# Kernel tuning notes

Hardware: AMD Instinct MI355X
Metric: run time of the kernel (lower is better)

Reference implementation:

```python
import jax, jax.numpy as jnp
import numpy as np

EMBED_DIM = 1024
BATCH = 4
SEQ = 2048


def setup_inputs() -> dict:
    key = jax.random.key(0)
    ks = jax.random.split(key, 9)
    E = EMBED_DIM
    s = 1.0 / np.sqrt(E)
    inp = {
        "x": jax.random.normal(ks[0], (BATCH, SEQ, E), dtype=jnp.float32),
        "Wq": jax.random.uniform(ks[1], (E, E), jnp.float32, -s, s),
        "bq": jax.random.uniform(ks[2], (E,), jnp.float32, -s, s),
        "Wk": jax.random.uniform(ks[3], (E, E), jnp.float32, -s, s),
        "bk": jax.random.uniform(ks[4], (E,), jnp.float32, -s, s),
        "Wv": jax.random.uniform(ks[5], (E, E), jnp.float32, -s, s),
        "bv": jax.random.uniform(ks[6], (E,), jnp.float32, -s, s),
        "Wo": jax.random.uniform(ks[7], (E, E), jnp.float32, -s, s),
        "bo": jax.random.uniform(ks[8], (E,), jnp.float32, -s, s),
    }
    return inp


def reference(x, Wq, bq, Wk, bk, Wv, bv, Wo, bo):
    # x: [B, S, E]. Single-head attention over full embed_dim.
    scale = x.shape[-1] ** -0.5
    q = jnp.einsum("bse,ef->bsf", x, Wq.T) + bq
    k = jnp.einsum("bse,ef->bsf", x, Wk.T) + bk
    v = jnp.einsum("bse,ef->bsf", x, Wv.T) + bv
    scores = jnp.einsum("bqe,bke->bqk", q, k) * scale  # [B, S, S]
    attn = jax.nn.softmax(scores, axis=-1)             # dropout p=0 -> identity
    out = jnp.einsum("bqk,bke->bqe", attn, v)
    return jnp.einsum("bse,ef->bsf", out, Wo.T) + bo
```

## Files before the change

### kernel.cpp

```cpp
#include <hip/hip_runtime.h>
#include <hip/hip_bf16.h>


typedef __bf16 bf16_t;
typedef __bf16 bf16x8 __attribute__((ext_vector_type(8)));
typedef __bf16 bf16x4 __attribute__((ext_vector_type(4)));
typedef float  f32x16 __attribute__((ext_vector_type(16)));
typedef float  f32x4  __attribute__((ext_vector_type(4)));

__device__ __forceinline__ void async_copy16(const void* g, void* l) {
  __builtin_amdgcn_global_load_lds(
      (const __attribute__((address_space(1))) void*)g,
      (__attribute__((address_space(3))) void*)l, 16, 0, 0);
}

__device__ __forceinline__ void wg_barrier() {
  asm volatile("" ::: "memory");
  __builtin_amdgcn_s_barrier();
  asm volatile("" ::: "memory");
}

#define LGKM(n)                                                  \
  do {                                                           \
    asm volatile("s_waitcnt lgkmcnt(" #n ")" ::: "memory");      \
    __builtin_amdgcn_sched_barrier(0);                           \
  } while (0)

#define VM(n) asm volatile("s_waitcnt vmcnt(" #n ")" ::: "memory")

__device__ __forceinline__ unsigned lds_addr(const void* p) {
  return (unsigned)(unsigned long long)(__attribute__((address_space(3))) const void*)p;
}

__device__ __forceinline__ bf16x8 ds_read128(const bf16_t* p) {
  bf16x8 r;
  asm volatile("ds_read_b128 %0, %1" : "=v"(r) : "v"(lds_addr(p)));
  return r;
}

__device__ __forceinline__ f32x4 mfma16(bf16x8 a, bf16x8 b, f32x4 c) {
  return __builtin_amdgcn_mfma_f32_16x16x32_bf16(a, b, c, 0, 0, 0);
}

__device__ __forceinline__ void store_out(float* p, float v)  { *p = v; }
__device__ __forceinline__ void store_out(bf16_t* p, float v) { *p = (bf16_t)v; }

#define BM 128
#define BN 128
#define BKT 64

#define G_AQ(i, ro, bb, co)                                                   \
  acc[(ro) + (i)][(co) + 0] = mfma16(a[i][0], bb[0][0], acc[(ro) + (i)][(co) + 0]); \
  acc[(ro) + (i)][(co) + 1] = mfma16(a[i][0], bb[1][0], acc[(ro) + (i)][(co) + 1]); \
  acc[(ro) + (i)][(co) + 0] = mfma16(a[i][1], bb[0][1], acc[(ro) + (i)][(co) + 0]); \
  acc[(ro) + (i)][(co) + 1] = mfma16(a[i][1], bb[1][1], acc[(ro) + (i)][(co) + 1]);

#define G_BQ(j, bb, co)                                              \
  acc[0][(co) + (j)] = mfma16(a[0][0], bb[j][0], acc[0][(co) + (j)]); \
  acc[1][(co) + (j)] = mfma16(a[1][0], bb[j][0], acc[1][(co) + (j)]); \
  acc[2][(co) + (j)] = mfma16(a[2][0], bb[j][0], acc[2][(co) + (j)]); \
  acc[3][(co) + (j)] = mfma16(a[3][0], bb[j][0], acc[3][(co) + (j)]); \
  acc[0][(co) + (j)] = mfma16(a[0][1], bb[j][1], acc[0][(co) + (j)]); \
  acc[1][(co) + (j)] = mfma16(a[1][1], bb[j][1], acc[1][(co) + (j)]); \
  acc[2][(co) + (j)] = mfma16(a[2][1], bb[j][1], acc[2][(co) + (j)]); \
  acc[3][(co) + (j)] = mfma16(a[3][1], bb[j][1], acc[3][(co) + (j)]);

template <typename OutT, int NBIAS>
__global__ __launch_bounds__(512, 2) void gemm256_bt(
    const bf16_t* __restrict__ A, const bf16_t* __restrict__ B,
    OutT* __restrict__ C,
    const float* __restrict__ b0, const float* __restrict__ b1,
    const float* __restrict__ b2,
    int M, int N, int K, int lda, int ldb, int ldc, float scale,
    long long strideA, long long strideB, long long strideC) {
  const int z = blockIdx.z;
  A += (long long)z * strideA;
  B += (long long)z * strideB;
  C += (long long)z * strideC;

  int bx = blockIdx.x, by = blockIdx.y;
  {
    const int GX  = gridDim.x;
    const int id  = by * GX + bx;
    const int per = GX * 8;
    const int grp = id / per;
    const int rem = id - grp * per;
    by = grp * 8 + (rem & 7);
    bx = rem >> 3;
  }

  __shared__ __align__(16) bf16_t As[2 * 256 * 64];
  __shared__ __align__(16) bf16_t Bs[2 * 256 * 64];

  const int t    = threadIdx.x;
  const int lane = t & 63;
  const int w    = t >> 6;
  const int wm   = w & 1;
  const int wn   = w >> 1;
  const int g    = lane >> 4;
  const int l7   = lane & 7;
  const int r15  = lane & 15;
  const int tileM = by * 256;
  const int tileN = bx * 256;

  const int row0 = t >> 3;
  const int gcc  = (t & 7) ^ (row0 & 7);
  const int dstb = (t & ~63) * 8;

  const int sw0 = ((0 + g) ^ l7) * 8;
  const int sw1 = ((4 + g) ^ l7) * 8;
  const int aRow = (wm * 128 + r15) * 64;
  const int bRow = (wn * 64 + r15) * 64;

  const int NT = K >> 6;

  f32x4 acc[8][4] = {};

  auto stageA = [&](int kt, int h) {
    const int cb = (kt & 1) * 16384;
    const bf16_t* src =
        A + (long long)(tileM + h * 128 + row0) * lda + kt * 64 + gcc * 8;
    bf16_t* dst = &As[cb + h * 8192 + dstb];
    async_copy16(src, dst);
    async_copy16(src + (long long)64 * lda, dst + 4096);
  };
  auto stageB = [&](int kt, int h) {
    const int cb = (kt & 1) * 16384;
    const bf16_t* src =
        B + (long long)(tileN + h * 128 + row0) * ldb + kt * 64 + gcc * 8;
    bf16_t* dst = &Bs[cb + h * 8192 + dstb];
    async_copy16(src, dst);
    async_copy16(src + (long long)64 * ldb, dst + 4096);
  };

  stageA(0, 0); stageA(0, 1); stageB(0, 0); stageB(0, 1);
  VM(0);
  wg_barrier();

  bf16x8 a[4][2], P[2][2], Q[2][2];
#pragma unroll
  for (int j = 0; j < 2; ++j) {
    P[j][0] = ds_read128(&Bs[bRow + j * 1024 + sw0]);
    P[j][1] = ds_read128(&Bs[bRow + j * 1024 + sw1]);
  }

  auto tile_step = [&](int kt, bf16x8 (&bc)[2][2], bf16x8 (&bq)[2][2]) {
    const int cb = (kt & 1) * 16384;
    const int kn = kt + 1;
    const bf16_t* Ab = &As[cb + aRow];
    const bf16_t* Bb = &Bs[cb + bRow];

#pragma unroll
    for (int i = 0; i < 4; ++i) {
      a[i][0] = ds_read128(Ab + i * 1024 + sw0);
      a[i][1] = ds_read128(Ab + i * 1024 + sw1);
    }
    if (kn < NT) { stageB(kn, 0); stageB(kn, 1); }
    __builtin_amdgcn_s_setprio(1);
    LGKM(6);
    G_AQ(0, 0, bc, 0)
    LGKM(4);
    G_AQ(1, 0, bc, 0)
    LGKM(2);
    G_AQ(2, 0, bc, 0)
    LGKM(0);
    G_AQ(3, 0, bc, 0)
    __builtin_amdgcn_s_setprio(0);

#pragma unroll
    for (int j = 0; j < 2; ++j) {
      bq[j][0] = ds_read128(Bb + 2048 + j * 1024 + sw0);
      bq[j][1] = ds_read128(Bb + 2048 + j * 1024 + sw1);
    }
    if (kn < NT) { stageA(kn, 0); stageA(kn, 1); }
    __builtin_amdgcn_s_setprio(1);
    LGKM(2);
    G_BQ(0, bq, 2)
    LGKM(0);
    G_BQ(1, bq, 2)
    __builtin_amdgcn_s_setprio(0);

#pragma unroll
    for (int i = 0; i < 4; ++i) {
      a[i][0] = ds_read128(Ab + 4096 + i * 1024 + sw0);
      a[i][1] = ds_read128(Ab + 4096 + i * 1024 + sw1);
    }
    __builtin_amdgcn_s_setprio(1);
    LGKM(6);
    G_AQ(0, 4, bq, 2)
    LGKM(4);
    G_AQ(1, 4, bq, 2)
    LGKM(2);
    G_AQ(2, 4, bq, 2)
    LGKM(0);
    G_AQ(3, 4, bq, 2)
    __builtin_amdgcn_s_setprio(0);
    VM(0);
    wg_barrier();

    if (kn < NT) {
      const bf16_t* Bn = &Bs[(kn & 1) * 16384 + bRow];
#pragma unroll
      for (int j = 0; j < 2; ++j) {
        bq[j][0] = ds_read128(Bn + j * 1024 + sw0);
        bq[j][1] = ds_read128(Bn + j * 1024 + sw1);
      }
    }
    __builtin_amdgcn_s_setprio(1);
    G_AQ(0, 4, bc, 0)
    G_AQ(1, 4, bc, 0)
    G_AQ(2, 4, bc, 0)
    G_AQ(3, 4, bc, 0)
    __builtin_amdgcn_s_setprio(0);
  };

  for (int kt = 0; kt < NT; kt += 2) {
    tile_step(kt,     P, Q);
    tile_step(kt + 1, Q, P);
  }

  float bvv[4];
#pragma unroll
  for (int j = 0; j < 4; ++j) {
    const int col = tileN + wn * 64 + j * 16 + r15;
    float bv = 0.f;
    if (NBIAS == 1) bv = b0[col];
    if (NBIAS == 3) {
      const float* bp = col < 1024 ? b0 : (col < 2048 ? b1 : b2);
      bv = bp[col & 1023];
    }
    bvv[j] = bv;
  }
#pragma unroll
  for (int i = 0; i < 8; ++i) {
#pragma unroll
    for (int r = 0; r < 4; ++r) {
      const long long row = tileM + wm * 128 + i * 16 + g * 4 + r;
      OutT* Crow = C + row * ldc + tileN + wn * 64 + r15;
#pragma unroll
      for (int j = 0; j < 4; ++j)
        store_out(Crow + j * 16, acc[i][j][r] * scale + bvv[j]);
    }
  }
}

template <typename OutT, int NBIAS>
__global__ __launch_bounds__(256) void gemm_bt(
    const bf16_t* __restrict__ A, const bf16_t* __restrict__ B,
    OutT* __restrict__ C,
    const float* __restrict__ b0, const float* __restrict__ b1,
    const float* __restrict__ b2,
    int M, int N, int K, int lda, int ldb, int ldc, float scale,
    long long strideA, long long strideB, long long strideC) {
  const int z = blockIdx.z;
  A += (long long)z * strideA;
  B += (long long)z * strideB;
  C += (long long)z * strideC;

  int bx = blockIdx.x, by = blockIdx.y;
  {
    const int GX  = gridDim.x;
    const int id  = by * GX + bx;
    const int per = GX * 8;
    const int grp = id / per;
    const int rem = id - grp * per;
    by = grp * 8 + (rem & 7);
    bx = rem >> 3;
  }

  __shared__ __align__(16) bf16_t As[BM * BKT];
  __shared__ __align__(16) bf16_t Bs[BN * BKT];

  const int t    = threadIdx.x;
  const int lane = t & 63;
  const int w    = t >> 6;
  const int wm   = w & 1;
  const int wn   = w >> 1;
  const int tileM = by * BM;
  const int tileN = bx * BN;

  f32x16 acc[2][2] = {};

  for (int k0 = 0; k0 < K; k0 += BKT) {
#pragma unroll
    for (int i = 0; i < 4; ++i) {
      const int c   = t + 256 * i;
      const int row = c >> 3;
      const int cc  = c & 7;
      const int gcc = cc ^ (row & 7);
      const int ldsbase = ((t & ~63) + 256 * i) * 8;
      async_copy16(A + (long long)(tileM + row) * lda + k0 + gcc * 8, &As[ldsbase]);
      async_copy16(B + (long long)(tileN + row) * ldb + k0 + gcc * 8, &Bs[ldsbase]);
    }
    __syncthreads();

#pragma unroll
    for (int s = 0; s < 4; ++s) {
      const int kc = s + 4 * (lane >> 5);
      bf16x8 af[2], bfr[2];
#pragma unroll
      for (int ti = 0; ti < 2; ++ti) {
        const int row = wm * 64 + ti * 32 + (lane & 31);
        af[ti] = *(const bf16x8*)&As[row * BKT + ((kc ^ (row & 7)) * 8)];
      }
#pragma unroll
      for (int tj = 0; tj < 2; ++tj) {
        const int row = wn * 64 + tj * 32 + (lane & 31);
        bfr[tj] = *(const bf16x8*)&Bs[row * BKT + ((kc ^ (row & 7)) * 8)];
      }
#pragma unroll
      for (int ti = 0; ti < 2; ++ti)
#pragma unroll
        for (int tj = 0; tj < 2; ++tj)
          acc[ti][tj] = __builtin_amdgcn_mfma_f32_32x32x16_bf16(
              af[ti], bfr[tj], acc[ti][tj], 0, 0, 0);
    }
    __syncthreads();
  }

#pragma unroll
  for (int tj = 0; tj < 2; ++tj) {
    const int col = tileN + wn * 64 + tj * 32 + (lane & 31);
    float bv = 0.f;
    if (NBIAS == 1) bv = b0[col];
    if (NBIAS == 3) {
      const float* bp = col < 1024 ? b0 : (col < 2048 ? b1 : b2);
      bv = bp[col & 1023];
    }
#pragma unroll
    for (int ti = 0; ti < 2; ++ti) {
      const int rowb = tileM + wm * 64 + ti * 32 + 4 * (lane >> 5);
#pragma unroll
      for (int r = 0; r < 16; ++r) {
        const int row = rowb + (r & 3) + 8 * (r >> 2);
        store_out(&C[(long long)row * ldc + col], acc[ti][tj][r] * scale + bv);
      }
    }
  }
}

__global__ __launch_bounds__(256) void cast_all(
    const float4* __restrict__ w0, const float4* __restrict__ w1,
    const float4* __restrict__ w2, const float4* __restrict__ w3,
    const float4* __restrict__ x,
    bf16x4* __restrict__ d0, bf16x4* __restrict__ d1,
    bf16x4* __restrict__ d2, bf16x4* __restrict__ d3,
    bf16x4* __restrict__ xdst) {
  const int N4W = 1 << 18;
  const int id = blockIdx.x * 256 + threadIdx.x;
  const float4* src;
  bf16x4* dst;
  if (id < 4 * N4W) {
    const int z = id >> 18;
    const int i = id & (N4W - 1);
    src = (z == 0 ? w0 : z == 1 ? w1 : z == 2 ? w2 : w3) + i;
    dst = (z == 0 ? d0 : z == 1 ? d1 : z == 2 ? d2 : d3) + i;
  } else {
    const int i = id - 4 * N4W;
    src = x + i;
    dst = xdst + i;
  }
  const float4 v = *src;
  bf16x4 o;
  o[0] = (bf16_t)v.x; o[1] = (bf16_t)v.y; o[2] = (bf16_t)v.z; o[3] = (bf16_t)v.w;
  *dst = o;
}

__global__ __launch_bounds__(256) void bias_v(
    const bf16_t* __restrict__ WkT, const float* __restrict__ bq,
    float* __restrict__ v) {
  const int wv   = threadIdx.x >> 6;
  const int lane = threadIdx.x & 63;
  const int j    = blockIdx.x * 4 + wv;
  const bf16x8* row = (const bf16x8*)(WkT + (long long)j * 1024);
  float acc = 0.f;
#pragma unroll
  for (int h = 0; h < 2; ++h) {
    const bf16x8 w8 = row[lane * 2 + h];
#pragma unroll
    for (int e = 0; e < 8; ++e)
      acc += (float)w8[e] * bq[lane * 16 + h * 8 + e];
  }
#pragma unroll
  for (int off = 32; off > 0; off >>= 1) acc += __shfl_xor(acc, off);
  if (lane == 0) v[j] = acc;
}

__global__ __launch_bounds__(256) void transpose_bf16(
    const bf16_t* __restrict__ in, bf16_t* __restrict__ out, int R, int C,
    int ldin, long long sIn, long long sOut) {
  in  += (long long)blockIdx.z * sIn;
  out += (long long)blockIdx.z * sOut;
  __shared__ bf16_t tile[32][33];
  const int tx = threadIdx.x, ty = threadIdx.y;
  const int x = blockIdx.x * 32 + tx;
  const int y0 = blockIdx.y * 32;
#pragma unroll
  for (int j = 0; j < 32; j += 8)
    tile[ty + j][tx] = in[(long long)(y0 + ty + j) * ldin + x];
  __syncthreads();
  const int x2 = y0 + tx;
  const int y2 = blockIdx.x * 32;
#pragma unroll
  for (int j = 0; j < 32; j += 8)
    out[(long long)(y2 + ty + j) * R + x2] = tile[tx][ty + j];
}

__global__ __launch_bounds__(256) void softmax_rows(
    const bf16_t* __restrict__ S, bf16_t* __restrict__ P, int cols) {
  const long long row = blockIdx.x;
  const bf16x8* inp = (const bf16x8*)(S + row * cols);
  bf16x8* outp      = (bf16x8*)(P + row * cols);
  const int t = threadIdx.x;
  const int w = t >> 6, lane = t & 63;

  const bf16x8 v = inp[t];
  float f[8];
#pragma unroll
  for (int j = 0; j < 8; ++j) f[j] = (float)v[j];

  float m = f[0];
#pragma unroll
  for (int j = 1; j < 8; ++j) m = fmaxf(m, f[j]);
#pragma unroll
  for (int off = 32; off > 0; off >>= 1) m = fmaxf(m, __shfl_xor(m, off));

  __shared__ float red[8];
  if (lane == 0) red[w] = m;
  __syncthreads();
  m = fmaxf(fmaxf(red[0], red[1]), fmaxf(red[2], red[3]));

  float e[8], sum = 0.f;
#pragma unroll
  for (int j = 0; j < 8; ++j) { e[j] = __expf(f[j] - m); sum += e[j]; }
#pragma unroll
  for (int off = 32; off > 0; off >>= 1) sum += __shfl_xor(sum, off);
  if (lane == 0) red[4 + w] = sum;
  __syncthreads();
  sum = red[4] + red[5] + red[6] + red[7];

  const float inv = 1.f / sum;
  bf16x8 o;
#pragma unroll
  for (int j = 0; j < 8; ++j) o[j] = (bf16_t)(e[j] * inv);
  outp[t] = o;
}

extern "C" void kernel_launch(void* const* d_in, const int* in_sizes, int n_in,
                              void* d_out, int out_size, void* d_ws, size_t ws_size,
                              hipStream_t stream) {
  const int E = 1024, S = 2048, B = 4;
  const int BS = B * S;

  const float* x  = (const float*)d_in[0];
  const float* Wq = (const float*)d_in[1];
  const float* bq = (const float*)d_in[2];
  const float* Wk = (const float*)d_in[3];
  const float* bk = (const float*)d_in[4];
  const float* Wv = (const float*)d_in[5];
  const float* bv = (const float*)d_in[6];
  const float* Wo = (const float*)d_in[7];
  const float* bo = (const float*)d_in[8];
  float* out = (float*)d_out;
  (void)bk; (void)Wk;

  char* w = (char*)d_ws;
  const size_t MB = 1ull << 20;
  bf16_t* Wqb  = (bf16_t*)(w + 0 * MB);
  bf16_t* Wkb  = Wqb + E * E;
  bf16_t* Wob  = (bf16_t*)(w + 4 * MB);
  float*  vb   = (float*)(w + 6 * MB);
  bf16_t* xb   = (bf16_t*)(w + 8 * MB);
  bf16_t* QVb  = (bf16_t*)(w + 24 * MB);
  bf16_t* WqTb = (bf16_t*)(w + 56 * MB);
  bf16_t* WkTb = WqTb + E * E;
  bf16_t* Wqv  = (bf16_t*)(w + 60 * MB);
  bf16_t* Wvb  = Wqv + E * E;
  bf16_t* VTb  = (bf16_t*)(w + 72 * MB);
  bf16_t* Sb   = (bf16_t*)(w + 88 * MB);
  bf16_t* Pb   = (bf16_t*)(w + 8 * MB);
  bf16_t* Ob   = (bf16_t*)(w + 40 * MB);

  {
    const int totalBlocks = ((4 << 18) + (1 << 21)) / 256;
    cast_all<<<totalBlocks, 256, 0, stream>>>(
        (const float4*)Wq, (const float4*)Wk, (const float4*)Wv,
        (const float4*)Wo, (const float4*)x,
        (bf16x4*)Wqb, (bf16x4*)Wkb, (bf16x4*)Wvb, (bf16x4*)Wob, (bf16x4*)xb);
  }

  transpose_bf16<<<dim3(E / 32, E / 32, 2), dim3(32, 8), 0, stream>>>(
      Wqb, WqTb, E, E, E, (long long)E * E, (long long)E * E);

  bias_v<<<256, 256, 0, stream>>>(WkTb, bq, vb);

  gemm_bt<bf16_t, 0><<<dim3(E / BN, E / BM, 1), 256, 0, stream>>>(
      WkTb, WqTb, Wqv, nullptr, nullptr, nullptr,
      E, E, E, E, E, E, 1.f, 0, 0, 0);

  gemm256_bt<bf16_t, 3><<<dim3(2 * E / 256, BS / 256, 1), 512, 0, stream>>>(
      xb, Wqv, QVb, vb, bv, bv,
      BS, 2 * E, E, E, E, 2 * E, 1.f, 0, 0, 0);

  transpose_bf16<<<dim3(E / 32, S / 32, B), dim3(32, 8), 0, stream>>>(
      QVb + E, VTb, S, E, 2 * E, (long long)S * 2 * E, (long long)E * S);

  gemm256_bt<bf16_t, 0><<<dim3(S / 256, S / 256, B), 512, 0, stream>>>(
      QVb, xb, Sb, nullptr, nullptr, nullptr,
      S, S, E, 2 * E, E, S, 0.03125f,
      (long long)S * 2 * E, (long long)S * E, (long long)S * S);

  softmax_rows<<<BS, 256, 0, stream>>>(Sb, Pb, S);

  gemm_bt<bf16_t, 0><<<dim3(E / BN, S / BM, B), 256, 0, stream>>>(
      Pb, VTb, Ob, nullptr, nullptr, nullptr,
      S, E, S, S, S, E, 1.f,
      (long long)S * S, (long long)E * S, (long long)S * E);

  gemm_bt<float, 1><<<dim3(E / BN, BS / BM, 1), 256, 0, stream>>>(
      Ob, Wob, out, bo, nullptr, nullptr,
      BS, E, E, E, E, E, 1.f, 0, 0, 0);
}
```

Baseline: 285.6 us.

## Add 256x128 double-buffered MFMA GEMM for PV and output projection

Adds a new 512-thread GEMM kernel with a 256x128 output tile, double-buffered async global-to-LDS loads, swizzled LDS reads, and interleaved MFMA with lgkmcnt waits. It also remaps blocks in groups of 8 rows for L2 locality. The P·V and output-projection GEMMs now use it instead of the older 256-thread kernel. The aim is more data reuse per tile and better overlap of loads with MFMA. The cost is higher register and LDS pressure from launch_bounds(512,2), and fewer blocks in the grid.

```diff
diff --git a/kernel.cpp b/kernel.cpp
--- a/kernel.cpp
+++ b/kernel.cpp
@@ -236,6 +236,194 @@
 #pragma unroll
     for (int r = 0; r < 4; ++r) {
       const long long row = tileM + wm * 128 + i * 16 + g * 4 + r;
+      OutT* Crow = C + row * ldc + tileN + wn * 64 + r15;
+#pragma unroll
+      for (int j = 0; j < 4; ++j)
+        store_out(Crow + j * 16, acc[i][j][r] * scale + bvv[j]);
+    }
+  }
+}
+
+template <typename OutT, int NBIAS>
+__global__ __launch_bounds__(512, 2) void gemm128n_bt(
+    const bf16_t* __restrict__ A, const bf16_t* __restrict__ B,
+    OutT* __restrict__ C,
+    const float* __restrict__ b0,
+    int M, int N, int K, int lda, int ldb, int ldc, float scale,
+    long long strideA, long long strideB, long long strideC) {
+  const int z = blockIdx.z;
+  A += (long long)z * strideA;
+  B += (long long)z * strideB;
+  C += (long long)z * strideC;
+
+  int bx = blockIdx.x, by = blockIdx.y;
+  {
+    const int GX  = gridDim.x;
+    const int id  = by * GX + bx;
+    const int per = GX * 8;
+    const int grp = id / per;
+    const int rem = id - grp * per;
+    by = grp * 8 + (rem & 7);
+    bx = rem >> 3;
+  }
+
+  __shared__ __align__(16) bf16_t As[2 * 256 * 64];
+  __shared__ __align__(16) bf16_t Bs[2 * 128 * 64];
+
+  const int t    = threadIdx.x;
+  const int lane = t & 63;
+  const int w    = t >> 6;
+  const int wm   = w & 3;
+  const int wn   = w >> 2;
+  const int g    = lane >> 4;
+  const int l7   = lane & 7;
+  const int r15  = lane & 15;
+  const int tileM = by * 256;
+  const int tileN = bx * 128;
+
+  const int row0 = t >> 3;
+  const int gcc  = (t & 7) ^ (row0 & 7);
+  const int dstb = (t & ~63) * 8;
+
+  const int sw0 = ((0 + g) ^ l7) * 8;
+  const int sw1 = ((4 + g) ^ l7) * 8;
+  const int aRow = (wm * 64 + r15) * 64;
+  const int bRow = (wn * 64 + r15) * 64;
+
+  const int NT = K >> 6;
+
+  f32x4 acc[4][4] = {};
+
+  auto stageA = [&](int kt, int h) {
+    const int cb = (kt & 1) * 16384;
+    const bf16_t* src =
+        A + (long long)(tileM + h * 128 + row0) * lda + kt * 64 + gcc * 8;
+    bf16_t* dst = &As[cb + h * 8192 + dstb];
+    async_copy16(src, dst);
+    async_copy16(src + (long long)64 * lda, dst + 4096);
+  };
+  auto stageB = [&](int kt) {
+    const int cb = (kt & 1) * 8192;
+    const bf16_t* src =
+        B + (long long)(tileN + row0) * ldb + kt * 64 + gcc * 8;
+    bf16_t* dst = &Bs[cb + dstb];
+    async_copy16(src, dst);
+    async_copy16(src + (long long)64 * ldb, dst + 4096);
+  };
+
+  stageA(0, 0); stageA(0, 1); stageB(0);
+  VM(0);
+  wg_barrier();
+
+  bf16x8 a[2][2], P[2][2], Q[2][2];
+#pragma unroll
+  for (int j = 0; j < 2; ++j) {
+    P[j][0] = ds_read128(&Bs[bRow + j * 1024 + sw0]);
+    P[j][1] = ds_read128(&Bs[bRow + j * 1024 + sw1]);
+  }
+
+  auto tile_step = [&](int kt, bf16x8 (&bc)[2][2], bf16x8 (&bq)[2][2]) {
+    const int cb = (kt & 1) * 16384;
+    const int kn = kt + 1;
+    const bf16_t* Ab = &As[cb + aRow];
+    const bf16_t* Bb = &Bs[(kt & 1) * 8192 + bRow];
+
+    a[0][0] = ds_read128(Ab + sw0);
+    a[0][1] = ds_read128(Ab + sw1);
+    a[1][0] = ds_read128(Ab + 1024 + sw0);
+    a[1][1] = ds_read128(Ab + 1024 + sw1);
+    if (kn < NT) stageB(kn);
+    __builtin_amdgcn_s_setprio(1);
+    LGKM(3);
+    acc[0][0] = mfma16(a[0][0], bc[0][0], acc[0][0]);
+    acc[0][1] = mfma16(a[0][0], bc[1][0], acc[0][1]);
+    LGKM(2);
+    acc[0][0] = mfma16(a[0][1], bc[0][1], acc[0][0]);
+    acc[0][1] = mfma16(a[0][1], bc[1][1], acc[0][1]);
+    LGKM(1);
+    acc[1][0] = mfma16(a[1][0], bc[0][0], acc[1][0]);
+    acc[1][1] = mfma16(a[1][0], bc[1][0], acc[1][1]);
+    LGKM(0);
+    acc[1][0] = mfma16(a[1][1], bc[0][1], acc[1][0]);
+    acc[1][1] = mfma16(a[1][1], bc[1][1], acc[1][1]);
+    __builtin_amdgcn_s_setprio(0);
+
+    bq[0][0] = ds_read128(Bb + 2048 + sw0);
+    bq[0][1] = ds_read128(Bb + 2048 + sw1);
+    bq[1][0] = ds_read128(Bb + 3072 + sw0);
+    bq[1][1] = ds_read128(Bb + 3072 + sw1);
+    if (kn < NT) { stageA(kn, 0); stageA(kn, 1); }
+    __builtin_amdgcn_s_setprio(1);
+    LGKM(3);
+    acc[0][2] = mfma16(a[0][0], bq[0][0], acc[0][2]);
+    acc[1][2] = mfma16(a[1][0], bq[0][0], acc[1][2]);
+    LGKM(2);
+    acc[0][2] = mfma16(a[0][1], bq[0][1], acc[0][2]);
+    acc[1][2] = mfma16(a[1][1], bq[0][1], acc[1][2]);
+    LGKM(1);
+    acc[0][3] = mfma16(a[0][0], bq[1][0], acc[0][3]);
+    acc[1][3] = mfma16(a[1][0], bq[1][0], acc[1][3]);
+    LGKM(0);
+    acc[0][3] = mfma16(a[0][1], bq[1][1], acc[0][3]);
+    acc[1][3] = mfma16(a[1][1], bq[1][1], acc[1][3]);
+    __builtin_amdgcn_s_setprio(0);
+
+    a[0][0] = ds_read128(Ab + 2048 + sw0);
+    a[0][1] = ds_read128(Ab + 2048 + sw1);
+    a[1][0] = ds_read128(Ab + 3072 + sw0);
+    a[1][1] = ds_read128(Ab + 3072 + sw1);
+    __builtin_amdgcn_s_setprio(1);
+    LGKM(3);
+    acc[2][2] = mfma16(a[0][0], bq[0][0], acc[2][2]);
+    acc[2][3] = mfma16(a[0][0], bq[1][0], acc[2][3]);
+    LGKM(2);
+    acc[2][2] = mfma16(a[0][1], bq[0][1], acc[2][2]);
+    acc[2][3] = mfma16(a[0][1], bq[1][1], acc[2][3]);
+    LGKM(1);
+    acc[3][2] = mfma16(a[1][0], bq[0][0], acc[3][2]);
+    acc[3][3] = mfma16(a[1][0], bq[1][0], acc[3][3]);
+    LGKM(0);
+    acc[3][2] = mfma16(a[1][1], bq[0][1], acc[3][2]);
+    acc[3][3] = mfma16(a[1][1], bq[1][1], acc[3][3]);
+    __builtin_amdgcn_s_setprio(0);
+    VM(0);
+    wg_barrier();
+
+    if (kn < NT) {
+      const bf16_t* Bn = &Bs[(kn & 1) * 8192 + bRow];
+      bq[0][0] = ds_read128(Bn + sw0);
+      bq[0][1] = ds_read128(Bn + sw1);
+      bq[1][0] = ds_read128(Bn + 1024 + sw0);
+      bq[1][1] = ds_read128(Bn + 1024 + sw1);
+    }
+    __builtin_amdgcn_s_setprio(1);
+    acc[2][0] = mfma16(a[0][0], bc[0][0], acc[2][0]);
+    acc[2][0] = mfma16(a[0][1], bc[0][1], acc[2][0]);
+    acc[2][1] = mfma16(a[0][0], bc[1][0], acc[2][1]);
+    acc[2][1] = mfma16(a[0][1], bc[1][1], acc[2][1]);
+    acc[3][0] = mfma16(a[1][0], bc[0][0], acc[3][0]);
+    acc[3][0] = mfma16(a[1][1], bc[0][1], acc[3][0]);
+    acc[3][1] = mfma16(a[1][0], bc[1][0], acc[3][1]);
+    acc[3][1] = mfma16(a[1][1], bc[1][1], acc[3][1]);
+    __builtin_amdgcn_s_setprio(0);
+  };
+
+  for (int kt = 0; kt < NT; kt += 2) {
+    tile_step(kt,     P, Q);
+    tile_step(kt + 1, Q, P);
+  }
+
+  float bvv[4];
+#pragma unroll
+  for (int j = 0; j < 4; ++j) {
+    const int col = tileN + wn * 64 + j * 16 + r15;
+    bvv[j] = (NBIAS == 1) ? b0[col] : 0.f;
+  }
+#pragma unroll
+  for (int i = 0; i < 4; ++i) {
+#pragma unroll
+    for (int r = 0; r < 4; ++r) {
+      const long long row = tileM + wm * 64 + i * 16 + g * 4 + r;
       OutT* Crow = C + row * ldc + tileN + wn * 64 + r15;
 #pragma unroll
       for (int j = 0; j < 4; ++j)
@@ -512,12 +700,12 @@
 
   softmax_rows<<<BS, 256, 0, stream>>>(Sb, Pb, S);
 
-  gemm_bt<bf16_t, 0><<<dim3(E / BN, S / BM, B), 256, 0, stream>>>(
-      Pb, VTb, Ob, nullptr, nullptr, nullptr,
+  gemm128n_bt<bf16_t, 0><<<dim3(E / 128, S / 256, B), 512, 0, stream>>>(
+      Pb, VTb, Ob, nullptr,
       S, E, S, S, S, E, 1.f,
       (long long)S * S, (long long)E * S, (long long)S * E);
 
-  gemm_bt<float, 1><<<dim3(E / BN, BS / BM, 1), 256, 0, stream>>>(
-      Ob, Wob, out, bo, nullptr, nullptr,
+  gemm128n_bt<float, 1><<<dim3(E / 128, BS / 256, 1), 512, 0, stream>>>(
+      Ob, Wob, out, bo,
       BS, E, E, E, E, E, 1.f, 0, 0, 0);
 }
```

After: 281.7 us. About the same (-1.4%).
